# Kernel tuning notes

Measured on AMD Instinct MI355X. Metric: run time of the kernel, lower is better.

The kernel has to match this reference:

```python
import jax, jax.numpy as jnp
import numpy as np

B, S, D, H = 2, 2048, 1024, 16
DK = D // H
NEG = -1000000000.0


def setup_inputs() -> dict:
    key = jax.random.key(0)
    ks = jax.random.split(key, 12)
    s = 1.0 / np.sqrt(D)
    return {
        "Q": jax.random.normal(ks[0], (B, S, D), jnp.float32),
        "K": jax.random.normal(ks[1], (B, S, D), jnp.float32),
        "V": jax.random.normal(ks[2], (B, S, D), jnp.float32),
        "attn_mask": jnp.zeros((B, S, S), jnp.bool_),
        "WQ_w": jax.random.normal(ks[3], (D, D), jnp.float32) * s,
        "WQ_b": jnp.zeros((D,), jnp.float32),
        "WK_w": jax.random.normal(ks[4], (D, D), jnp.float32) * s,
        "WK_b": jnp.zeros((D,), jnp.float32),
        "WV_w": jax.random.normal(ks[5], (D, D), jnp.float32) * s,
        "WV_b": jnp.zeros((D,), jnp.float32),
        "fc_w": jax.random.normal(ks[6], (D, D), jnp.float32) * s,
        "fc_b": jnp.zeros((D,), jnp.float32),
    }


def reference(Q, K, V, attn_mask, WQ_w, WQ_b, WK_w, WK_b, WV_w, WV_b, fc_w, fc_b):
    b = Q.shape[0]
    # linear projections (torch Linear: x @ W^T + b), split heads -> [b, h, s, dk]
    q = (Q @ WQ_w.T + WQ_b).reshape(b, -1, H, DK).transpose(0, 2, 1, 3)
    k = (K @ WK_w.T + WK_b).reshape(b, -1, H, DK).transpose(0, 2, 1, 3)
    v = (V @ WV_w.T + WV_b).reshape(b, -1, H, DK).transpose(0, 2, 1, 3)
    # scaled dot-product attention with masked_fill
    scores = jnp.einsum("bhqd,bhkd->bhqk", q, k) / jnp.sqrt(jnp.float32(DK))
    scores = jnp.where(attn_mask[:, None, :, :], NEG, scores)
    attn_weights = jax.nn.softmax(scores, axis=-1)  # dropout p=0 -> identity
    attn = jnp.einsum("bhqk,bhkd->bhqd", attn_weights, v)
    attn = attn.transpose(0, 2, 1, 3).reshape(b, -1, H * DK)
    output = attn @ fc_w.T + fc_b
    return output, attn_weights
```

## Files before the change

kernel.cpp:

```cpp
#include <hip/hip_runtime.h>
#include <cstdint>
#include <cstddef>

constexpr int CB = 2;
constexpr int CS = 2048;
constexpr int CD = 1024;
constexpr int CH = 16;
constexpr int CDK = 64;
constexpr float NEGV = -1000000000.0f;
constexpr float QSCALE = 0.18033688011112042f;

typedef __bf16 bf16x8 __attribute__((ext_vector_type(8)));
typedef float f32x4 __attribute__((ext_vector_type(4)));
typedef unsigned short u16x8 __attribute__((ext_vector_type(8)));
typedef unsigned short u16x4 __attribute__((ext_vector_type(4)));

static __device__ __forceinline__ unsigned short f2bf(float x) {
  unsigned int u = __float_as_uint(x);
  u += 0x7fffu + ((u >> 16) & 1u);
  return (unsigned short)(u >> 16);
}
static __device__ __forceinline__ bf16x8 bc8(u16x8 u) {
  return __builtin_bit_cast(bf16x8, u);
}
static __device__ __forceinline__ f32x4 mfma16(bf16x8 a, bf16x8 b, f32x4 c) {
  return __builtin_amdgcn_mfma_f32_16x16x32_bf16(a, b, c, 0, 0, 0);
}

struct CvtArgs {
  const float* src[7];
  unsigned short* dst[7];
  int n4[7];
};

__global__ __launch_bounds__(256) void cvt_all(CvtArgs a) {
  const int r = blockIdx.y;
  const float* __restrict__ in = a.src[r];
  unsigned short* __restrict__ out = a.dst[r];
  const int n4 = a.n4[r];
  const int stride = gridDim.x * 256;
  for (int i = blockIdx.x * 256 + threadIdx.x; i < n4; i += stride) {
    float4 v = reinterpret_cast<const float4*>(in)[i];
    u16x4 o;
    o[0] = f2bf(v.x); o[1] = f2bf(v.y); o[2] = f2bf(v.z); o[3] = f2bf(v.w);
    reinterpret_cast<u16x4*>(out)[i] = o;
  }
}

constexpr int GK = 1024, GNT = GK / 32;

struct QKVArgs {
  const unsigned short* X[3];
  const unsigned short* W[3];
  const float* bias[3];
  unsigned short* out[3];
  float osc[3];
};

template <int BN, typename EPI>
__device__ __forceinline__ void gemm_body(const unsigned short* __restrict__ X,
                                          const unsigned short* __restrict__ Wt,
                                          EPI epi) {
  __shared__ unsigned short lA[2][128 * 32];
  __shared__ unsigned short lB[2][BN * 32];
  const int tid = threadIdx.x, lane = tid & 63, wid = tid >> 6;
  const int fr = lane & 15, fc = lane >> 4;
  const int mbase = blockIdx.y * 128, nbase = blockIdx.x * BN;
  const int wm = (wid & 1) * 64, wn = (wid >> 1) * (BN / 2);

  const int srow = lane >> 2;
  const int sslot = (lane & 3) ^ (srow & 3);
  const int cA = wid * 2;
  const unsigned short* a0 = X + (size_t)(mbase + cA * 16 + srow) * GK + sslot * 8;
  const unsigned short* b0;
  if constexpr (BN == 128) b0 = Wt + (size_t)(nbase + cA * 16 + srow) * GK + sslot * 8;
  else                     b0 = Wt + (size_t)(nbase + wid * 16 + srow) * GK + sslot * 8;

  auto stage = [&](int buf, int k0) {
#pragma unroll
    for (int c = 0; c < 2; ++c)
      __builtin_amdgcn_global_load_lds(
          (const __attribute__((address_space(1))) void*)(a0 + (size_t)c * 16 * GK + k0),
          (__attribute__((address_space(3))) void*)((char*)&lA[buf][0] + (cA + c) * 1024), 16, 0, 0);
    if constexpr (BN == 128) {
#pragma unroll
      for (int c = 0; c < 2; ++c)
        __builtin_amdgcn_global_load_lds(
            (const __attribute__((address_space(1))) void*)(b0 + (size_t)c * 16 * GK + k0),
            (__attribute__((address_space(3))) void*)((char*)&lB[buf][0] + (cA + c) * 1024), 16, 0, 0);
    } else {
      __builtin_amdgcn_global_load_lds(
          (const __attribute__((address_space(1))) void*)(b0 + k0),
          (__attribute__((address_space(3))) void*)((char*)&lB[buf][0] + wid * 1024), 16, 0, 0);
    }
  };

  constexpr int NJ = BN / 32;
  f32x4 acc[4][NJ] = {};
  stage(0, 0);
  __syncthreads();
  for (int t = 0; t < GNT; ++t) {
    if (t + 1 < GNT) stage((t + 1) & 1, (t + 1) * 32);
    const int buf = t & 1;
    bf16x8 af[4], bfv[NJ];
#pragma unroll
    for (int i = 0; i < 4; ++i) {
      const int row = wm + i * 16 + fr;
      af[i] = bc8(*reinterpret_cast<const u16x8*>(&lA[buf][row * 32 + ((fc ^ (row & 3)) * 8)]));
    }
#pragma unroll
    for (int j = 0; j < NJ; ++j) {
      const int row = wn + j * 16 + fr;
      bfv[j] = bc8(*reinterpret_cast<const u16x8*>(&lB[buf][row * 32 + ((fc ^ (row & 3)) * 8)]));
    }
#pragma unroll
    for (int i = 0; i < 4; ++i)
#pragma unroll
      for (int j = 0; j < NJ; ++j)
        acc[i][j] = mfma16(af[i], bfv[j], acc[i][j]);
    __syncthreads();
  }

#pragma unroll
  for (int j = 0; j < NJ; ++j) {
    const int colb = nbase + wn + j * 16 + fr;
#pragma unroll
    for (int i = 0; i < 4; ++i) {
#pragma unroll
      for (int r = 0; r < 4; ++r) {
        const int rowb = mbase + wm + i * 16 + fc * 4 + r;
        epi(rowb, colb, acc[i][j][r]);
      }
    }
  }
}

__global__ __launch_bounds__(256, 3) void gemm_qkv(QKVArgs a) {
  const int z = blockIdx.z;
  const float* bias = a.bias[z];
  unsigned short* out = a.out[z];
  const float osc = a.osc[z];
  gemm_body<128>(a.X[z], a.W[z], [&](int rowb, int colb, float av) {
    const float v = (av + bias[colb]) * osc;
    const int bb = rowb >> 11, sr = rowb & (CS - 1);
    const int hh = colb >> 6, cc = colb & (CDK - 1);
    const size_t bh = (size_t)bb * CH + hh;
    if (z == 0) {
      out[(bh * CS + sr) * CDK + cc] = f2bf(v);
    } else if (z == 1) {
      const int kt = sr >> 6, ww = sr & 63, g = ww >> 4, fr2 = ww & 15;
      const int half = cc >> 5, fc2 = (cc >> 3) & 3, zz = cc & 7;
      out[(bh * 256 + kt * 8 + g * 2 + half) * 512 + (fc2 * 16 + fr2) * 8 + zz] = f2bf(v);
    } else {
      const int kt = sr >> 6, kk = sr & 63;
      const int c = kk >> 5, k32 = kk & 31;
      const int fcv = (k32 >> 2) & 3;
      const int zv = ((k32 >> 4) << 2) | (k32 & 3);
      const int g = cc >> 4, fr2 = cc & 15;
      out[(bh * 256 + kt * 8 + c * 4 + g) * 512 + (fr2 + 16 * fcv) * 8 + zv] = f2bf(v);
    }
  });
}

__global__ __launch_bounds__(256) void gemm_fc(const unsigned short* __restrict__ X,
                                               const unsigned short* __restrict__ Wt,
                                               const float* __restrict__ bias,
                                               float* __restrict__ out) {
  gemm_body<64>(X, Wt, [&](int rowb, int colb, float av) {
    out[(size_t)rowb * CD + colb] = av + bias[colb];
  });
}

__global__ __launch_bounds__(256, 3) void attn_fused(const unsigned short* __restrict__ qh,
                                                     const unsigned short* __restrict__ kT,
                                                     const unsigned short* __restrict__ vT,
                                                     const unsigned char* __restrict__ mask,
                                                     float* __restrict__ attnw,
                                                     unsigned short* __restrict__ attn_pre) {
  const int tid = threadIdx.x, lane = tid & 63, wid = tid >> 6;
  const int bid = blockIdx.x;
  const int swz = (bid & 7) * 128 + (bid >> 3);
  const int qt = swz & 31, hh = (swz >> 5) & 15, b = swz >> 9;
  const int bh = b * CH + hh;
  const int qw = qt * 64 + wid * 16;
  const int fr = lane & 15, fc = lane >> 4;

  const unsigned short* qp = qh + ((size_t)bh * CS + qw + fr) * CDK + fc * 8;
  const bf16x8 aq0 = bc8(*reinterpret_cast<const u16x8*>(qp));
  const bf16x8 aq1 = bc8(*reinterpret_cast<const u16x8*>(qp + 32));

  const unsigned short* kbase = kT + (size_t)bh * 131072 + lane * 8;
  const unsigned short* vbase = vT + (size_t)bh * 131072 + lane * 8;

  const unsigned char* mrow = mask + ((size_t)b * CS + qw + (lane >> 2)) * CS + (lane & 3) * 16;
  unsigned int dirtybits = 0;
#pragma unroll 4
  for (int kt = 0; kt < 32; ++kt) {
    const uint4 mv = *reinterpret_cast<const uint4*>(mrow + kt * 64);
    if (__ballot((mv.x | mv.y | mv.z | mv.w) != 0)) dirtybits |= (1u << kt);
  }

  u16x8 kreg[8];
  auto loadK = [&](int kt) {
    const unsigned short* p = kbase + (size_t)kt * 4096;
#pragma unroll
    for (int f = 0; f < 8; ++f) kreg[f] = *reinterpret_cast<const u16x8*>(p + f * 512);
  };
  auto qk = [&](f32x4 (&sf)[4]) {
#pragma unroll
    for (int g = 0; g < 4; ++g) {
      f32x4 a = {0.f, 0.f, 0.f, 0.f};
      a = mfma16(bc8(kreg[2 * g]), aq0, a);
      a = mfma16(bc8(kreg[2 * g + 1]), aq1, a);
      sf[g] = a;
    }
  };
  const unsigned char* mq = mask + ((size_t)b * CS + qw + fr) * CS + fc * 4;
  auto maskfix = [&](f32x4 (&sf)[4], int kt) {
#pragma unroll
    for (int g = 0; g < 4; ++g) {
      const uchar4 m4 = *reinterpret_cast<const uchar4*>(mq + kt * 64 + g * 16);
      if (m4.x) sf[g][0] = NEGV;
      if (m4.y) sf[g][1] = NEGV;
      if (m4.z) sf[g][2] = NEGV;
      if (m4.w) sf[g][3] = NEGV;
    }
  };

  float lsum = 0.f;
  loadK(0);
  for (int kt = 0; kt < 32; ++kt) {
    f32x4 sf[4];
    qk(sf);
    loadK(kt + 1 < 32 ? kt + 1 : 0);
    if ((dirtybits >> kt) & 1u) maskfix(sf, kt);
#pragma unroll
    for (int g = 0; g < 4; ++g)
      lsum += (exp2f(sf[g][0]) + exp2f(sf[g][1])) + (exp2f(sf[g][2]) + exp2f(sf[g][3]));
  }
  lsum += __shfl_xor(lsum, 16);
  lsum += __shfl_xor(lsum, 32);
  const float linv = 1.0f / lsum;

  f32x4 o[4] = {};
  u16x8 vreg[8];
  auto loadV = [&](int kt) {
    const unsigned short* p = vbase + (size_t)kt * 4096;
#pragma unroll
    for (int f = 0; f < 8; ++f) vreg[f] = *reinterpret_cast<const u16x8*>(p + f * 512);
  };

  float* wrow = attnw + ((size_t)bh * CS + qw + fr) * CS + fc * 4;

  loadK(0);
  for (int kt = 0; kt < 32; ++kt) {
    loadV(kt);

    f32x4 sf[4];
    qk(sf);
    loadK(kt + 1 < 32 ? kt + 1 : 0);
    if ((dirtybits >> kt) & 1u) maskfix(sf, kt);

#pragma unroll
    for (int g = 0; g < 4; ++g)
#pragma unroll
      for (int r = 0; r < 4; ++r) sf[g][r] = exp2f(sf[g][r]) * linv;

#pragma unroll
    for (int g = 0; g < 4; ++g)
      __builtin_nontemporal_store(sf[g], reinterpret_cast<f32x4*>(wrow + kt * 64 + g * 16));

    bf16x8 pa[2];
#pragma unroll
    for (int c = 0; c < 2; ++c) {
      unsigned int w0, w1, w2, w3;
      asm("v_cvt_pk_bf16_f32 %0, %1, %2" : "=v"(w0) : "v"(sf[2 * c][0]), "v"(sf[2 * c][1]));
      asm("v_cvt_pk_bf16_f32 %0, %1, %2" : "=v"(w1) : "v"(sf[2 * c][2]), "v"(sf[2 * c][3]));
      asm("v_cvt_pk_bf16_f32 %0, %1, %2" : "=v"(w2) : "v"(sf[2 * c + 1][0]), "v"(sf[2 * c + 1][1]));
      asm("v_cvt_pk_bf16_f32 %0, %1, %2" : "=v"(w3) : "v"(sf[2 * c + 1][2]), "v"(sf[2 * c + 1][3]));
      uint4 uw = {w0, w1, w2, w3};
      pa[c] = __builtin_bit_cast(bf16x8, uw);
    }
#pragma unroll
    for (int g = 0; g < 4; ++g) o[g] = mfma16(pa[0], bc8(vreg[g]), o[g]);
#pragma unroll
    for (int g = 0; g < 4; ++g) o[g] = mfma16(pa[1], bc8(vreg[4 + g]), o[g]);
  }

#pragma unroll
  for (int g = 0; g < 4; ++g)
#pragma unroll
    for (int r = 0; r < 4; ++r) {
      const int q = qw + fc * 4 + r;
      attn_pre[(((size_t)b * CS + q) * CH + hh) * CDK + g * 16 + fr] = f2bf(o[g][r]);
    }
}

extern "C" void kernel_launch(void* const* d_in, const int* in_sizes, int n_in,
                              void* d_out, int out_size, void* d_ws, size_t ws_size,
                              hipStream_t stream) {
  (void)in_sizes; (void)n_in; (void)out_size; (void)ws_size;

  const float* Qf = (const float*)d_in[0];
  const float* Kf = (const float*)d_in[1];
  const float* Vf = (const float*)d_in[2];
  const unsigned char* mask = (const unsigned char*)d_in[3];
  const float* WQw = (const float*)d_in[4];
  const float* WQb = (const float*)d_in[5];
  const float* WKw = (const float*)d_in[6];
  const float* WKb = (const float*)d_in[7];
  const float* WVw = (const float*)d_in[8];
  const float* WVb = (const float*)d_in[9];
  const float* fcw = (const float*)d_in[10];
  const float* fcb = (const float*)d_in[11];

  float* out0 = (float*)d_out;
  float* attnw = out0 + (size_t)CB * CS * CD;

  char* w = (char*)d_ws;
  unsigned short* Qb = (unsigned short*)(w);
  unsigned short* Kb = (unsigned short*)(w + 8388608);
  unsigned short* Vb = (unsigned short*)(w + 2 * 8388608);
  unsigned short* Wqb = (unsigned short*)(w + 3 * 8388608);
  unsigned short* Wkb = Wqb + 1048576;
  unsigned short* Wvb = Wkb + 1048576;
  unsigned short* Wfb = Wvb + 1048576;
  unsigned short* qhp = (unsigned short*)(w + 3 * 8388608 + 4 * 2097152);
  unsigned short* kTp = qhp + 4194304;
  unsigned short* vTp = kTp + 4194304;
  unsigned short* apre = Qb;

  const int NELEM4 = (CB * CS * CD) / 4;
  const int WELEM4 = (CD * CD) / 4;

  CvtArgs ca;
  ca.src[0] = Qf;  ca.dst[0] = Qb;  ca.n4[0] = NELEM4;
  ca.src[1] = Kf;  ca.dst[1] = Kb;  ca.n4[1] = NELEM4;
  ca.src[2] = Vf;  ca.dst[2] = Vb;  ca.n4[2] = NELEM4;
  ca.src[3] = WQw; ca.dst[3] = Wqb; ca.n4[3] = WELEM4;
  ca.src[4] = WKw; ca.dst[4] = Wkb; ca.n4[4] = WELEM4;
  ca.src[5] = WVw; ca.dst[5] = Wvb; ca.n4[5] = WELEM4;
  ca.src[6] = fcw; ca.dst[6] = Wfb; ca.n4[6] = WELEM4;
  cvt_all<<<dim3(512, 7), 256, 0, stream>>>(ca);

  QKVArgs qa;
  qa.X[0] = Qb;  qa.W[0] = Wqb; qa.bias[0] = WQb; qa.out[0] = qhp; qa.osc[0] = QSCALE;
  qa.X[1] = Kb;  qa.W[1] = Wkb; qa.bias[1] = WKb; qa.out[1] = kTp; qa.osc[1] = 1.0f;
  qa.X[2] = Vb;  qa.W[2] = Wvb; qa.bias[2] = WVb; qa.out[2] = vTp; qa.osc[2] = 1.0f;
  gemm_qkv<<<dim3(CD / 128, (CB * CS) / 128, 3), 256, 0, stream>>>(qa);

  attn_fused<<<dim3(1024), 256, 0, stream>>>(qhp, kTp, vTp, mask, attnw, apre);

  gemm_fc<<<dim3(CD / 64, (CB * CS) / 128), 256, 0, stream>>>(apre, Wfb, fcb, out0);
}
```

Before: 262.7 us.

## Split softmax row-sum pass into a separate key-parallel kernel

The softmax denominator pass moves out of the fused attention kernel into its own kernel. That kernel splits the key dimension four ways across waves and runs 4096 blocks with higher occupancy, writing partial sums to workspace. The second kernel reads and adds the four partials before computing the weights and the PV product. The aim is more parallelism for the denominator phase, at the cost of an extra launch, recomputing QK^T in a separate kernel, and a small workspace round trip.

Result: slower. 377.8 us (+43.8%).

```diff
diff --git a/kernel.cpp b/kernel.cpp
--- a/kernel.cpp
+++ b/kernel.cpp
@@ -171,10 +171,78 @@
   });
 }
 
-__global__ __launch_bounds__(256, 3) void attn_fused(const unsigned short* __restrict__ qh,
+__global__ __launch_bounds__(256, 5) void attn_pass1(const unsigned short* __restrict__ qh,
+                                                     const unsigned short* __restrict__ kT,
+                                                     const unsigned char* __restrict__ mask,
+                                                     float* __restrict__ lsum) {
+  const int tid = threadIdx.x, lane = tid & 63, kq = tid >> 6;
+  const int bid = blockIdx.x;
+  const int swz = (bid & 7) * 512 + (bid >> 3);
+  const int q16 = swz & 127, hh = (swz >> 7) & 15, b = swz >> 11;
+  const int bh = b * CH + hh;
+  const int qw = q16 * 16;
+  const int fr = lane & 15, fc = lane >> 4;
+
+  const unsigned short* qp = qh + ((size_t)bh * CS + qw + fr) * CDK + fc * 8;
+  const bf16x8 aq0 = bc8(*reinterpret_cast<const u16x8*>(qp));
+  const bf16x8 aq1 = bc8(*reinterpret_cast<const u16x8*>(qp + 32));
+
+  const unsigned short* kbase = kT + (size_t)bh * 131072 + lane * 8;
+  const int kt0 = kq * 8;
+
+  const unsigned char* mrow = mask + ((size_t)b * CS + qw + (lane >> 2)) * CS + (lane & 3) * 16;
+  unsigned int dirty = 0;
+#pragma unroll
+  for (int i = 0; i < 8; ++i) {
+    const uint4 mv = *reinterpret_cast<const uint4*>(mrow + (kt0 + i) * 64);
+    if (__ballot((mv.x | mv.y | mv.z | mv.w) != 0)) dirty |= (1u << i);
+  }
+
+  u16x8 kreg[8];
+  auto loadK = [&](int kt) {
+    const unsigned short* p = kbase + (size_t)kt * 4096;
+#pragma unroll
+    for (int f = 0; f < 8; ++f) kreg[f] = *reinterpret_cast<const u16x8*>(p + f * 512);
+  };
+  const unsigned char* mq = mask + ((size_t)b * CS + qw + fr) * CS + fc * 4;
+
+  float ls = 0.f;
+  loadK(kt0);
+  for (int i = 0; i < 8; ++i) {
+    const int kt = kt0 + i;
+    f32x4 sf[4];
+#pragma unroll
+    for (int g = 0; g < 4; ++g) {
+      f32x4 a = {0.f, 0.f, 0.f, 0.f};
+      a = mfma16(bc8(kreg[2 * g]), aq0, a);
+      a = mfma16(bc8(kreg[2 * g + 1]), aq1, a);
+      sf[g] = a;
+    }
+    loadK(i + 1 < 8 ? kt + 1 : kt0);
+    if ((dirty >> i) & 1u) {
+#pragma unroll
+      for (int g = 0; g < 4; ++g) {
+        const uchar4 m4 = *reinterpret_cast<const uchar4*>(mq + kt * 64 + g * 16);
+        if (m4.x) sf[g][0] = NEGV;
+        if (m4.y) sf[g][1] = NEGV;
+        if (m4.z) sf[g][2] = NEGV;
+        if (m4.w) sf[g][3] = NEGV;
+      }
+    }
+#pragma unroll
+    for (int g = 0; g < 4; ++g)
+      ls += (exp2f(sf[g][0]) + exp2f(sf[g][1])) + (exp2f(sf[g][2]) + exp2f(sf[g][3]));
+  }
+  ls += __shfl_xor(ls, 16);
+  ls += __shfl_xor(ls, 32);
+  if (lane < 16) lsum[((size_t)kq * 32 + bh) * CS + qw + fr] = ls;
+}
+
+__global__ __launch_bounds__(256, 3) void attn_pass2(const unsigned short* __restrict__ qh,
                                                      const unsigned short* __restrict__ kT,
                                                      const unsigned short* __restrict__ vT,
                                                      const unsigned char* __restrict__ mask,
+                                                     const float* __restrict__ lsum,
                                                      float* __restrict__ attnw,
                                                      unsigned short* __restrict__ attn_pre) {
   const int tid = threadIdx.x, lane = tid & 63, wid = tid >> 6;
@@ -192,6 +260,11 @@
   const unsigned short* kbase = kT + (size_t)bh * 131072 + lane * 8;
   const unsigned short* vbase = vT + (size_t)bh * 131072 + lane * 8;
 
+  float ls = 0.f;
+#pragma unroll
+  for (int kq = 0; kq < 4; ++kq) ls += lsum[((size_t)kq * 32 + bh) * CS + qw + fr];
+  const float linv = 1.0f / ls;
+
   const unsigned char* mrow = mask + ((size_t)b * CS + qw + (lane >> 2)) * CS + (lane & 3) * 16;
   unsigned int dirtybits = 0;
 #pragma unroll 4
@@ -226,21 +299,6 @@
       if (m4.w) sf[g][3] = NEGV;
     }
   };
-
-  float lsum = 0.f;
-  loadK(0);
-  for (int kt = 0; kt < 32; ++kt) {
-    f32x4 sf[4];
-    qk(sf);
-    loadK(kt + 1 < 32 ? kt + 1 : 0);
-    if ((dirtybits >> kt) & 1u) maskfix(sf, kt);
-#pragma unroll
-    for (int g = 0; g < 4; ++g)
-      lsum += (exp2f(sf[g][0]) + exp2f(sf[g][1])) + (exp2f(sf[g][2]) + exp2f(sf[g][3]));
-  }
-  lsum += __shfl_xor(lsum, 16);
-  lsum += __shfl_xor(lsum, 32);
-  const float linv = 1.0f / lsum;
 
   f32x4 o[4] = {};
   u16x8 vreg[8];
@@ -329,6 +387,7 @@
   unsigned short* kTp = qhp + 4194304;
   unsigned short* vTp = kTp + 4194304;
   unsigned short* apre = Qb;
+  float* lsum_ws = (float*)Kb;
 
   const int NELEM4 = (CB * CS * CD) / 4;
   const int WELEM4 = (CD * CD) / 4;
@@ -349,7 +408,8 @@
   qa.X[2] = Vb;  qa.W[2] = Wvb; qa.bias[2] = WVb; qa.out[2] = vTp; qa.osc[2] = 1.0f;
   gemm_qkv<<<dim3(CD / 128, (CB * CS) / 128, 3), 256, 0, stream>>>(qa);
 
-  attn_fused<<<dim3(1024), 256, 0, stream>>>(qhp, kTp, vTp, mask, attnw, apre);
+  attn_pass1<<<dim3(4096), 256, 0, stream>>>(qhp, kTp, mask, lsum_ws);
+  attn_pass2<<<dim3(1024), 256, 0, stream>>>(qhp, kTp, vTp, mask, lsum_ws, attnw, apre);
 
   gemm_fc<<<dim3(CD / 64, (CB * CS) / 128), 256, 0, stream>>>(apre, Wfb, fcb, out0);
 }
```

## Process two 16-row query tiles per wave to reuse K/V register loads

Applied to the files above, without the earlier changes.

Each wave in the fused attention kernel now handles 32 query rows (two 16-row halves) instead of 16. The K and V fragments loaded into registers each key tile are shared by both halves, which halves global K/V traffic per query row. The grid shrinks from 1024 to 512 blocks and the occupancy hint drops from 3 to 2 blocks per CU to make room for the extra registers. The trade-off is fewer waves available to hide latency; the kernel also writes a large fp32 attention-weights tensor, so it may be bound by stores rather than K/V loads.

Result: slower. 286.0 us (+8.9%).

```diff
diff --git a/kernel.cpp b/kernel.cpp
--- a/kernel.cpp
+++ b/kernel.cpp
@@ -171,7 +171,7 @@
   });
 }
 
-__global__ __launch_bounds__(256, 3) void attn_fused(const unsigned short* __restrict__ qh,
+__global__ __launch_bounds__(256, 2) void attn_fused(const unsigned short* __restrict__ qh,
                                                      const unsigned short* __restrict__ kT,
                                                      const unsigned short* __restrict__ vT,
                                                      const unsigned char* __restrict__ mask,
@@ -179,25 +179,32 @@
                                                      unsigned short* __restrict__ attn_pre) {
   const int tid = threadIdx.x, lane = tid & 63, wid = tid >> 6;
   const int bid = blockIdx.x;
-  const int swz = (bid & 7) * 128 + (bid >> 3);
-  const int qt = swz & 31, hh = (swz >> 5) & 15, b = swz >> 9;
+  const int swz = (bid & 7) * 64 + (bid >> 3);
+  const int qt = swz & 15, hh = (swz >> 4) & 15, b = swz >> 8;
   const int bh = b * CH + hh;
-  const int qw = qt * 64 + wid * 16;
+  const int qwA = qt * 128 + wid * 32;
+  const int qwB = qwA + 16;
   const int fr = lane & 15, fc = lane >> 4;
 
-  const unsigned short* qp = qh + ((size_t)bh * CS + qw + fr) * CDK + fc * 8;
-  const bf16x8 aq0 = bc8(*reinterpret_cast<const u16x8*>(qp));
-  const bf16x8 aq1 = bc8(*reinterpret_cast<const u16x8*>(qp + 32));
+  const unsigned short* qpA = qh + ((size_t)bh * CS + qwA + fr) * CDK + fc * 8;
+  const bf16x8 aqA0 = bc8(*reinterpret_cast<const u16x8*>(qpA));
+  const bf16x8 aqA1 = bc8(*reinterpret_cast<const u16x8*>(qpA + 32));
+  const unsigned short* qpB = qpA + 16 * CDK;
+  const bf16x8 aqB0 = bc8(*reinterpret_cast<const u16x8*>(qpB));
+  const bf16x8 aqB1 = bc8(*reinterpret_cast<const u16x8*>(qpB + 32));
 
   const unsigned short* kbase = kT + (size_t)bh * 131072 + lane * 8;
   const unsigned short* vbase = vT + (size_t)bh * 131072 + lane * 8;
 
-  const unsigned char* mrow = mask + ((size_t)b * CS + qw + (lane >> 2)) * CS + (lane & 3) * 16;
+  const unsigned char* mrowA = mask + ((size_t)b * CS + qwA + (lane >> 2)) * CS + (lane & 3) * 16;
+  const unsigned char* mrowB = mrowA + (size_t)16 * CS;
   unsigned int dirtybits = 0;
 #pragma unroll 4
   for (int kt = 0; kt < 32; ++kt) {
-    const uint4 mv = *reinterpret_cast<const uint4*>(mrow + kt * 64);
-    if (__ballot((mv.x | mv.y | mv.z | mv.w) != 0)) dirtybits |= (1u << kt);
+    const uint4 m0 = *reinterpret_cast<const uint4*>(mrowA + kt * 64);
+    const uint4 m1 = *reinterpret_cast<const uint4*>(mrowB + kt * 64);
+    if (__ballot((m0.x | m0.y | m0.z | m0.w | m1.x | m1.y | m1.z | m1.w) != 0))
+      dirtybits |= (1u << kt);
   }
 
   u16x8 kreg[8];
@@ -206,17 +213,18 @@
 #pragma unroll
     for (int f = 0; f < 8; ++f) kreg[f] = *reinterpret_cast<const u16x8*>(p + f * 512);
   };
-  auto qk = [&](f32x4 (&sf)[4]) {
+  auto qk = [&](const bf16x8 b0, const bf16x8 b1, f32x4 (&sf)[4]) {
 #pragma unroll
     for (int g = 0; g < 4; ++g) {
       f32x4 a = {0.f, 0.f, 0.f, 0.f};
-      a = mfma16(bc8(kreg[2 * g]), aq0, a);
-      a = mfma16(bc8(kreg[2 * g + 1]), aq1, a);
+      a = mfma16(bc8(kreg[2 * g]), b0, a);
+      a = mfma16(bc8(kreg[2 * g + 1]), b1, a);
       sf[g] = a;
     }
   };
-  const unsigned char* mq = mask + ((size_t)b * CS + qw + fr) * CS + fc * 4;
-  auto maskfix = [&](f32x4 (&sf)[4], int kt) {
+  const unsigned char* mqA = mask + ((size_t)b * CS + qwA + fr) * CS + fc * 4;
+  const unsigned char* mqB = mqA + (size_t)16 * CS;
+  auto maskfix = [&](f32x4 (&sf)[4], int kt, const unsigned char* mq) {
 #pragma unroll
     for (int g = 0; g < 4; ++g) {
       const uchar4 m4 = *reinterpret_cast<const uchar4*>(mq + kt * 64 + g * 16);
@@ -227,49 +235,45 @@
     }
   };
 
-  float lsum = 0.f;
+  float lsA = 0.f, lsB = 0.f;
   loadK(0);
   for (int kt = 0; kt < 32; ++kt) {
-    f32x4 sf[4];
-    qk(sf);
+    f32x4 sfA[4], sfB[4];
+    qk(aqA0, aqA1, sfA);
+    qk(aqB0, aqB1, sfB);
     loadK(kt + 1 < 32 ? kt + 1 : 0);
-    if ((dirtybits >> kt) & 1u) maskfix(sf, kt);
-#pragma unroll
-    for (int g = 0; g < 4; ++g)
-      lsum += (exp2f(sf[g][0]) + exp2f(sf[g][1])) + (exp2f(sf[g][2]) + exp2f(sf[g][3]));
-  }
-  lsum += __shfl_xor(lsum, 16);
-  lsum += __shfl_xor(lsum, 32);
-  const float linv = 1.0f / lsum;
-
-  f32x4 o[4] = {};
+    if ((dirtybits >> kt) & 1u) { maskfix(sfA, kt, mqA); maskfix(sfB, kt, mqB); }
+#pragma unroll
+    for (int g = 0; g < 4; ++g) {
+      lsA += (exp2f(sfA[g][0]) + exp2f(sfA[g][1])) + (exp2f(sfA[g][2]) + exp2f(sfA[g][3]));
+      lsB += (exp2f(sfB[g][0]) + exp2f(sfB[g][1])) + (exp2f(sfB[g][2]) + exp2f(sfB[g][3]));
+    }
+  }
+  lsA += __shfl_xor(lsA, 16);
+  lsA += __shfl_xor(lsA, 32);
+  lsB += __shfl_xor(lsB, 16);
+  lsB += __shfl_xor(lsB, 32);
+  const float linvA = 1.0f / lsA;
+  const float linvB = 1.0f / lsB;
+
+  f32x4 oA[4] = {}, oB[4] = {};
   u16x8 vreg[8];
   auto loadV = [&](int kt) {
     const unsigned short* p = vbase + (size_t)kt * 4096;
 #pragma unroll
     for (int f = 0; f < 8; ++f) vreg[f] = *reinterpret_cast<const u16x8*>(p + f * 512);
   };
-
-  float* wrow = attnw + ((size_t)bh * CS + qw + fr) * CS + fc * 4;
-
-  loadK(0);
-  for (int kt = 0; kt < 32; ++kt) {
-    loadV(kt);
-
-    f32x4 sf[4];
-    qk(sf);
-    loadK(kt + 1 < 32 ? kt + 1 : 0);
-    if ((dirtybits >> kt) & 1u) maskfix(sf, kt);
-
+  float* wrowA = attnw + ((size_t)bh * CS + qwA + fr) * CS + fc * 4;
+  float* wrowB = wrowA + (size_t)16 * CS;
+
+  auto half = [&](f32x4 (&sf)[4], const float linv, float* wrow, f32x4 (&o)[4], int kt) {
 #pragma unroll
     for (int g = 0; g < 4; ++g)
 #pragma unroll
       for (int r = 0; r < 4; ++r) sf[g][r] = exp2f(sf[g][r]) * linv;
-
 #pragma unroll
     for (int g = 0; g < 4; ++g)
       __builtin_nontemporal_store(sf[g], reinterpret_cast<f32x4*>(wrow + kt * 64 + g * 16));
-
     bf16x8 pa[2];
 #pragma unroll
     for (int c = 0; c < 2; ++c) {
@@ -285,14 +289,30 @@
     for (int g = 0; g < 4; ++g) o[g] = mfma16(pa[0], bc8(vreg[g]), o[g]);
 #pragma unroll
     for (int g = 0; g < 4; ++g) o[g] = mfma16(pa[1], bc8(vreg[4 + g]), o[g]);
+  };
+
+  loadK(0);
+  for (int kt = 0; kt < 32; ++kt) {
+    loadV(kt);
+
+    f32x4 sfA[4], sfB[4];
+    qk(aqA0, aqA1, sfA);
+    qk(aqB0, aqB1, sfB);
+    loadK(kt + 1 < 32 ? kt + 1 : 0);
+    if ((dirtybits >> kt) & 1u) { maskfix(sfA, kt, mqA); maskfix(sfB, kt, mqB); }
+
+    half(sfA, linvA, wrowA, oA, kt);
+    half(sfB, linvB, wrowB, oB, kt);
   }
 
 #pragma unroll
   for (int g = 0; g < 4; ++g)
 #pragma unroll
     for (int r = 0; r < 4; ++r) {
-      const int q = qw + fc * 4 + r;
-      attn_pre[(((size_t)b * CS + q) * CH + hh) * CDK + g * 16 + fr] = f2bf(o[g][r]);
+      const int qA = qwA + fc * 4 + r;
+      attn_pre[(((size_t)b * CS + qA) * CH + hh) * CDK + g * 16 + fr] = f2bf(oA[g][r]);
+      const int qB = qwB + fc * 4 + r;
+      attn_pre[(((size_t)b * CS + qB) * CH + hh) * CDK + g * 16 + fr] = f2bf(oB[g][r]);
     }
 }
 
@@ -349,7 +369,7 @@
   qa.X[2] = Vb;  qa.W[2] = Wvb; qa.bias[2] = WVb; qa.out[2] = vTp; qa.osc[2] = 1.0f;
   gemm_qkv<<<dim3(CD / 128, (CB * CS) / 128, 3), 256, 0, stream>>>(qa);
 
-  attn_fused<<<dim3(1024), 256, 0, stream>>>(qhp, kTp, vTp, mask, attnw, apre);
+  attn_fused<<<dim3(512), 256, 0, stream>>>(qhp, kTp, vTp, mask, attnw, apre);
 
   gemm_fc<<<dim3(CD / 64, (CB * CS) / 128), 256, 0, stream>>>(apre, Wfb, fcb, out0);
 }
```

## Precompute mask dirty-tile table in separate kernel, raise occupancy, add MFMA priority

Applied to the files above, without the earlier changes.

Moves the per-tile mask scan out of the attention kernel into a small mask_scan kernel that writes one 32-bit dirty bitmap per (batch, 64-row query tile), written into the now-unused K bf16 buffer. Before, each of the 16 head blocks re-read the same 64x2048 mask slab; now it is read once per query tile. The change also raises launch_bounds occupancy from 3 to 4 blocks, wraps MFMA sections in s_setprio, and drops the wasted K prefetch on the last iteration. The costs are an extra kernel launch and register pressure from the higher occupancy target.

Measured after the change: 256.1 us. -2.5%, faster.

```diff
diff --git a/kernel.cpp b/kernel.cpp
--- a/kernel.cpp
+++ b/kernel.cpp
@@ -45,6 +45,29 @@
     o[0] = f2bf(v.x); o[1] = f2bf(v.y); o[2] = f2bf(v.z); o[3] = f2bf(v.w);
     reinterpret_cast<u16x4*>(out)[i] = o;
   }
+}
+
+__global__ __launch_bounds__(256) void mask_scan(const unsigned char* __restrict__ mask,
+                                                 unsigned int* __restrict__ tab) {
+  __shared__ unsigned int w;
+  if (threadIdx.x == 0) w = 0;
+  __syncthreads();
+  const int b = blockIdx.y, qt = blockIdx.x;
+  const int t = threadIdx.x;
+  const int row = qt * 64 + (t >> 2);
+  const unsigned char* p = mask + ((size_t)b * CS + row) * CS + (t & 3) * 512;
+  unsigned int local = 0;
+#pragma unroll
+  for (int i = 0; i < 8; ++i) {
+    const uint4* q = reinterpret_cast<const uint4*>(p + i * 64);
+    const uint4 a = q[0], b4 = q[1], c = q[2], d = q[3];
+    if ((a.x | a.y | a.z | a.w | b4.x | b4.y | b4.z | b4.w |
+         c.x | c.y | c.z | c.w | d.x | d.y | d.z | d.w) != 0)
+      local |= 1u << ((t & 3) * 8 + i);
+  }
+  if (local) atomicOr(&w, local);
+  __syncthreads();
+  if (t == 0) tab[b * 32 + qt] = w;
 }
 
 constexpr int GK = 1024, GNT = GK / 32;
@@ -171,10 +194,11 @@
   });
 }
 
-__global__ __launch_bounds__(256, 3) void attn_fused(const unsigned short* __restrict__ qh,
+__global__ __launch_bounds__(256, 4) void attn_fused(const unsigned short* __restrict__ qh,
                                                      const unsigned short* __restrict__ kT,
                                                      const unsigned short* __restrict__ vT,
                                                      const unsigned char* __restrict__ mask,
+                                                     const unsigned int* __restrict__ dirtytab,
                                                      float* __restrict__ attnw,
                                                      unsigned short* __restrict__ attn_pre) {
   const int tid = threadIdx.x, lane = tid & 63, wid = tid >> 6;
@@ -185,6 +209,8 @@
   const int qw = qt * 64 + wid * 16;
   const int fr = lane & 15, fc = lane >> 4;
 
+  const unsigned int dirtybits = dirtytab[b * 32 + qt];
+
   const unsigned short* qp = qh + ((size_t)bh * CS + qw + fr) * CDK + fc * 8;
   const bf16x8 aq0 = bc8(*reinterpret_cast<const u16x8*>(qp));
   const bf16x8 aq1 = bc8(*reinterpret_cast<const u16x8*>(qp + 32));
@@ -192,14 +218,6 @@
   const unsigned short* kbase = kT + (size_t)bh * 131072 + lane * 8;
   const unsigned short* vbase = vT + (size_t)bh * 131072 + lane * 8;
 
-  const unsigned char* mrow = mask + ((size_t)b * CS + qw + (lane >> 2)) * CS + (lane & 3) * 16;
-  unsigned int dirtybits = 0;
-#pragma unroll 4
-  for (int kt = 0; kt < 32; ++kt) {
-    const uint4 mv = *reinterpret_cast<const uint4*>(mrow + kt * 64);
-    if (__ballot((mv.x | mv.y | mv.z | mv.w) != 0)) dirtybits |= (1u << kt);
-  }
-
   u16x8 kreg[8];
   auto loadK = [&](int kt) {
     const unsigned short* p = kbase + (size_t)kt * 4096;
@@ -207,6 +225,7 @@
     for (int f = 0; f < 8; ++f) kreg[f] = *reinterpret_cast<const u16x8*>(p + f * 512);
   };
   auto qk = [&](f32x4 (&sf)[4]) {
+    __builtin_amdgcn_s_setprio(1);
 #pragma unroll
     for (int g = 0; g < 4; ++g) {
       f32x4 a = {0.f, 0.f, 0.f, 0.f};
@@ -214,6 +233,7 @@
       a = mfma16(bc8(kreg[2 * g + 1]), aq1, a);
       sf[g] = a;
     }
+    __builtin_amdgcn_s_setprio(0);
   };
   const unsigned char* mq = mask + ((size_t)b * CS + qw + fr) * CS + fc * 4;
   auto maskfix = [&](f32x4 (&sf)[4], int kt) {
@@ -232,7 +252,7 @@
   for (int kt = 0; kt < 32; ++kt) {
     f32x4 sf[4];
     qk(sf);
-    loadK(kt + 1 < 32 ? kt + 1 : 0);
+    if (kt + 1 < 32) loadK(kt + 1);
     if ((dirtybits >> kt) & 1u) maskfix(sf, kt);
 #pragma unroll
     for (int g = 0; g < 4; ++g)
@@ -258,7 +278,7 @@
 
     f32x4 sf[4];
     qk(sf);
-    loadK(kt + 1 < 32 ? kt + 1 : 0);
+    if (kt + 1 < 32) loadK(kt + 1);
     if ((dirtybits >> kt) & 1u) maskfix(sf, kt);
 
 #pragma unroll
@@ -281,10 +301,12 @@
       uint4 uw = {w0, w1, w2, w3};
       pa[c] = __builtin_bit_cast(bf16x8, uw);
     }
+    __builtin_amdgcn_s_setprio(1);
 #pragma unroll
     for (int g = 0; g < 4; ++g) o[g] = mfma16(pa[0], bc8(vreg[g]), o[g]);
 #pragma unroll
     for (int g = 0; g < 4; ++g) o[g] = mfma16(pa[1], bc8(vreg[4 + g]), o[g]);
+    __builtin_amdgcn_s_setprio(0);
   }
 
 #pragma unroll
@@ -329,6 +351,7 @@
   unsigned short* kTp = qhp + 4194304;
   unsigned short* vTp = kTp + 4194304;
   unsigned short* apre = Qb;
+  unsigned int* dirtytab = (unsigned int*)Kb;
 
   const int NELEM4 = (CB * CS * CD) / 4;
   const int WELEM4 = (CD * CD) / 4;
@@ -349,7 +372,9 @@
   qa.X[2] = Vb;  qa.W[2] = Wvb; qa.bias[2] = WVb; qa.out[2] = vTp; qa.osc[2] = 1.0f;
   gemm_qkv<<<dim3(CD / 128, (CB * CS) / 128, 3), 256, 0, stream>>>(qa);
 
-  attn_fused<<<dim3(1024), 256, 0, stream>>>(qhp, kTp, vTp, mask, attnw, apre);
+  mask_scan<<<dim3(32, CB), 256, 0, stream>>>(mask, dirtytab);
+
+  attn_fused<<<dim3(1024), 256, 0, stream>>>(qhp, kTp, vTp, mask, dirtytab, attnw, apre);
 
   gemm_fc<<<dim3(CD / 64, (CB * CS) / 128), 256, 0, stream>>>(apre, Wfb, fcb, out0);
 }
```
